# Kernel tuning notes

Measured on AMD Instinct MI355X. Metric: run time of the kernel, lower is better.

## Reference

```python
import jax, jax.numpy as jnp
import numpy as np

DIM = 2048
NUM_HEADS = 16
HEAD_DIM = DIM // NUM_HEADS  # 128
LATENT = 512
THETA = 10000.0


def rotate_half(x):
    # interleaved rotate: (x0,x1,x2,x3,...) -> (-x1,x0,-x3,x2,...)
    x1 = x[..., ::2]
    x2 = x[..., 1::2]
    return jnp.stack((-x2, x1), axis=-1).reshape(x.shape)


def apply_rope(x, sin, cos):
    return x * cos + rotate_half(x) * sin


def setup_inputs() -> dict:
    key = jax.random.key(0)
    ks = jax.random.split(key, 6)
    s_in = 1.0 / np.sqrt(DIM)
    s_lat = 1.0 / np.sqrt(LATENT)
    x = jax.random.normal(ks[0], (2, 2048, DIM), dtype=jnp.float32)
    Wq = jax.random.normal(ks[1], (DIM, DIM), dtype=jnp.float32) * s_in
    Wdkv = jax.random.normal(ks[2], (DIM, 2 * LATENT), dtype=jnp.float32) * s_in
    Wuk = jax.random.normal(ks[3], (LATENT, DIM), dtype=jnp.float32) * s_lat
    Wuv = jax.random.normal(ks[4], (LATENT, DIM), dtype=jnp.float32) * s_lat
    Wo = jax.random.normal(ks[5], (DIM, DIM), dtype=jnp.float32) * s_in
    return {"x": x, "Wq": Wq, "Wdkv": Wdkv, "Wuk": Wuk, "Wuv": Wuv, "Wo": Wo}


def reference(x, Wq, Wdkv, Wuk, Wuv, Wo):
    b, s, _ = x.shape
    # q projection -> [b, h, s, hd]
    q = (x @ Wq).reshape(b, s, NUM_HEADS, HEAD_DIM).transpose(0, 2, 1, 3)
    # low-rank latent down-projection, then up-project K and V
    dkv = x @ Wdkv  # [b, s, 2*L]
    dk, dv = dkv[..., :LATENT], dkv[..., LATENT:]
    k = (dk @ Wuk).reshape(b, s, NUM_HEADS, HEAD_DIM).transpose(0, 2, 1, 3)
    v = (dv @ Wuv).reshape(b, s, NUM_HEADS, HEAD_DIM).transpose(0, 2, 1, 3)
    # RoPE cache (concatenated freqs, matching the torch module)
    inv_freq = 1.0 / (THETA ** (jnp.arange(0, HEAD_DIM, 2, dtype=jnp.float32) / HEAD_DIM))
    t = jnp.arange(s, dtype=jnp.float32)
    freqs = t[:, None] * inv_freq[None, :]          # [s, hd/2]
    emb = jnp.concatenate([freqs, freqs], axis=-1)  # [s, hd]
    sin, cos = jnp.sin(emb), jnp.cos(emb)
    q = apply_rope(q, sin, cos)
    k = apply_rope(k, sin, cos)
    # SDPA (no mask, no dropout): scale = 1/sqrt(head_dim)
    scores = jnp.einsum('bhqd,bhkd->bhqk', q, k) / jnp.sqrt(jnp.float32(HEAD_DIM))
    attn = jax.nn.softmax(scores, axis=-1)
    out = jnp.einsum('bhqk,bhkd->bhqd', attn, v)
    out = out.transpose(0, 2, 1, 3).reshape(b, s, DIM)
    return out @ Wo
```

## Files before the change

### kernel.cpp

```cpp
#include <hip/hip_runtime.h>
#include <hip/hip_bf16.h>
#include <stdint.h>

typedef __attribute__((ext_vector_type(8))) __bf16 bf16x8;
typedef __attribute__((ext_vector_type(4))) float f32x4;

__device__ __forceinline__ unsigned short f2bf(float f) {
  union { float f; unsigned u; } v; v.f = f;
  unsigned r = v.u + 0x7FFFu + ((v.u >> 16) & 1u);
  return (unsigned short)(r >> 16);
}

__device__ __forceinline__ float fast_exp2(float x) {
#if __has_builtin(__builtin_amdgcn_exp2f)
  return __builtin_amdgcn_exp2f(x);
#else
  return exp2f(x);
#endif
}

__device__ __forceinline__ void gload_lds16(const void* g, void* l) {
  __builtin_amdgcn_global_load_lds((const __attribute__((address_space(1))) void*)g,
                                   (__attribute__((address_space(3))) void*)l,
                                   16, 0, 0);
}

__global__ __launch_bounds__(256) void k_prep(
    const float* __restrict__ x, unsigned short* __restrict__ xb,
    const float* __restrict__ Wq, unsigned short* __restrict__ WqT,
    const float* __restrict__ Wdkv, unsigned short* __restrict__ WdkvT,
    const float* __restrict__ Wuk, unsigned short* __restrict__ WukT,
    const float* __restrict__ Wuv, unsigned short* __restrict__ WuvT,
    float* __restrict__ cosT, float* __restrict__ sinT) {
  const int bid = blockIdx.x;
  const int tid = threadIdx.x;
  if (bid < 8192) {
    int i = (bid * 256 + tid) * 4;
    float4 v = *reinterpret_cast<const float4*>(x + i);
    ushort4 o;
    o.x = f2bf(v.x); o.y = f2bf(v.y); o.z = f2bf(v.z); o.w = f2bf(v.w);
    *reinterpret_cast<ushort4*>(xb + i) = o;
    return;
  }
  if (bid >= 16384) {
    int idx = (bid - 16384) * 256 + tid;
    int t = idx >> 6, j = idx & 63;
    float inv = powf(10000.f, -(float)j / 64.f);
    float ang = (float)t * inv;
    cosT[idx] = cosf(ang);
    sinT[idx] = sinf(ang);
    return;
  }
  const float* in; unsigned short* out; int K, N, lid;
  if (bid < 12288)      { in = Wq;   out = WqT;   K = 2048; N = 2048; lid = bid - 8192; }
  else if (bid < 14336) { in = Wdkv; out = WdkvT; K = 2048; N = 1024; lid = bid - 12288; }
  else if (bid < 15360) { in = Wuk;  out = WukT;  K = 512;  N = 2048; lid = bid - 14336; }
  else                  { in = Wuv;  out = WuvT;  K = 512;  N = 2048; lid = bid - 15360; }
  const int ntx = N >> 5;
  const int nt = lid % ntx, kt = lid / ntx;
  __shared__ float t[32][33];
  const int tx = tid & 31, ty = tid >> 5;
#pragma unroll
  for (int i = 0; i < 4; i++)
    t[ty + i * 8][tx] = in[(size_t)(kt * 32 + ty + i * 8) * N + nt * 32 + tx];
  __syncthreads();
#pragma unroll
  for (int i = 0; i < 4; i++)
    out[(size_t)(nt * 32 + ty + i * 8) * K + kt * 32 + tx] = f2bf(t[tx][ty + i * 8]);
}

template <int EPI>
__global__ __launch_bounds__(256, 2) void k_gemm(
    const unsigned short* __restrict__ A, int lda,
    const unsigned short* __restrict__ BT, int ldb,
    void* __restrict__ Cout, void* __restrict__ Cout2, int M, int N, int K,
    const float* __restrict__ cosT, const float* __restrict__ sinT) {
  __shared__ __attribute__((aligned(16))) unsigned short As[128 * 64];
  __shared__ __attribute__((aligned(16))) unsigned short Bs[128 * 64];
  const int tid = threadIdx.x;

  if (EPI == 3 && blockIdx.y >= 32) {
    const float* Win = cosT;
    unsigned short* Wout = (unsigned short*)Cout2;
    float (*t)[33] = (float(*)[33])As;
    const int tx = tid & 31, ty = tid >> 5;
    const int lid = (blockIdx.y - 32) * gridDim.x + blockIdx.x;
    for (int it = 0; it < 128; ++it) {
      int tile = lid * 128 + it;
      int nt = tile & 63, kt2 = tile >> 6;
#pragma unroll
      for (int i = 0; i < 4; i++)
        t[ty + i * 8][tx] = Win[(size_t)(kt2 * 32 + ty + i * 8) * 2048 + nt * 32 + tx];
      __syncthreads();
#pragma unroll
      for (int i = 0; i < 4; i++)
        Wout[(size_t)(nt * 32 + ty + i * 8) * 2048 + kt2 * 32 + tx] = f2bf(t[tx][ty + i * 8]);
      __syncthreads();
    }
    return;
  }

  const int lane = tid & 63;
  const int w = tid >> 6;
  const int wr = w >> 1, wc = w & 1;

  const int nby = (EPI == 3) ? 32 : gridDim.y;
  const int nwg = gridDim.x * nby;
  const int cpx = nwg >> 3;
  int flat = blockIdx.y * gridDim.x + blockIdx.x;
  flat = (flat & 7) * cpx + (flat >> 3);
  const int m0 = (flat / gridDim.x) * 128, n0 = (flat % gridDim.x) * 128;

  f32x4 acc[4][4] = {};

  const int srow = w * 8 + (lane >> 3);
  const int sch = (lane & 7) * 8;
  const unsigned short* gA = A + (size_t)(m0 + srow) * lda + sch;
  const unsigned short* gB = BT + (size_t)(n0 + srow) * ldb + sch;
  unsigned short* lA = &As[srow * 64 + sch];
  unsigned short* lB = &Bs[srow * 64 + sch];

  for (int kt = 0; kt < K; kt += 64) {
    __syncthreads();
#pragma unroll
    for (int i = 0; i < 4; i++) {
      gload_lds16(gA + (size_t)(i * 32) * lda + kt, lA + i * 32 * 64);
      gload_lds16(gB + (size_t)(i * 32) * ldb + kt, lB + i * 32 * 64);
    }
    __syncthreads();
#pragma unroll
    for (int kk = 0; kk < 64; kk += 32) {
      bf16x8 af[4], bfr[4];
#pragma unroll
      for (int m = 0; m < 4; m++)
        af[m] = *reinterpret_cast<const bf16x8*>(&As[(wr * 64 + m * 16 + (lane & 15)) * 64 + kk + (lane >> 4) * 8]);
#pragma unroll
      for (int n = 0; n < 4; n++)
        bfr[n] = *reinterpret_cast<const bf16x8*>(&Bs[(wc * 64 + n * 16 + (lane & 15)) * 64 + kk + (lane >> 4) * 8]);
#pragma unroll
      for (int m = 0; m < 4; m++)
#pragma unroll
        for (int n = 0; n < 4; n++) {
          if (EPI == 3)
            acc[m][n] = __builtin_amdgcn_mfma_f32_16x16x32_bf16(bfr[n], af[m], acc[m][n], 0, 0, 0);
          else
            acc[m][n] = __builtin_amdgcn_mfma_f32_16x16x32_bf16(af[m], bfr[n], acc[m][n], 0, 0, 0);
        }
    }
  }

  const int rl = (lane >> 4) * 4;
  const int cl = lane & 15;
#pragma unroll
  for (int m = 0; m < 4; m++)
#pragma unroll
    for (int n = 0; n < 4; n++)
#pragma unroll
      for (int r = 0; r < 4; r++) {
        float v = acc[m][n][r];
        if (EPI == 4) {
          int gr = m0 + wr * 64 + m * 16 + rl + r;
          int gc = n0 + wc * 64 + n * 16 + cl;
          ((float*)Cout)[(size_t)gr * N + gc] = v;
        } else if (EPI == 1) {
          int gr = m0 + wr * 64 + m * 16 + rl + r;
          int gc = n0 + wc * 64 + n * 16 + cl;
          int b = gr >> 11, s = gr & 2047, h = gc >> 7, d = gc & 127;
          float p = __shfl_xor(v, 1);
          float c = cosT[s * 64 + (d & 63)];
          float sn = sinT[s * 64 + (d & 63)];
          v = v * c + ((d & 1) ? p : -p) * sn;
          ((unsigned short*)Cout)[((size_t)(b * 16 + h) * 2048 + s) * 128 + d] = f2bf(v);
        } else if (EPI == 5) {
          int gr = m0 + wr * 64 + m * 16 + rl + r;
          int gc = n0 + wc * 64 + n * 16 + cl;
          if (n0 < 2048) {
            int b = gr >> 11, s = gr & 2047, h = gc >> 7, d = gc & 127;
            float p = __shfl_xor(v, 1);
            float c = cosT[s * 64 + (d & 63)];
            float sn = sinT[s * 64 + (d & 63)];
            v = v * c + ((d & 1) ? p : -p) * sn;
            ((unsigned short*)Cout)[((size_t)(b * 16 + h) * 2048 + s) * 128 + d] = f2bf(v);
          } else {
            ((unsigned short*)Cout2)[(size_t)gr * 1024 + (gc - 2048)] = f2bf(v);
          }
        } else {
          int gd = n0 + wc * 64 + n * 16 + rl + r;
          int gs = m0 + wr * 64 + m * 16 + cl;
          int b = gs >> 11, s = gs & 2047, h = gd >> 7, d = gd & 127;
          ((unsigned short*)Cout)[((size_t)(b * 16 + h) * 128 + d) * 2048 + s] = f2bf(v);
        }
      }
}

__global__ __launch_bounds__(256, 2) void k_attn(
    const unsigned short* __restrict__ Q,
    const unsigned short* __restrict__ Kt,
    const unsigned short* __restrict__ Vt,
    unsigned short* __restrict__ O) {
  __shared__ __attribute__((aligned(16))) unsigned short Kls[2][64 * 128];
  __shared__ __attribute__((aligned(16))) unsigned short Vls[2][128 * 64];
  __shared__ __attribute__((aligned(16))) unsigned short Pls[128 * 64];
  const int flat = blockIdx.x + (blockIdx.y << 4);
  const int swz = (flat & 7) * 64 + (flat >> 3);
  const int qt = swz & 15, bh = swz >> 4;
  const int tid = threadIdx.x, lane = tid & 63, w = tid >> 6;
  const unsigned short* Qh = Q + (size_t)bh * 2048 * 128;
  const unsigned short* Kh = Kt + (size_t)bh * 2048 * 128;
  const unsigned short* Vh = Vt + (size_t)bh * 128 * 2048;
  const int q0 = qt * 128;

  bf16x8 qf[2][4];
#pragma unroll
  for (int m = 0; m < 2; m++)
#pragma unroll
    for (int kd = 0; kd < 4; kd++) {
      int row = q0 + w * 32 + m * 16 + (lane & 15);
      int k = kd * 32 + (lane >> 4) * 8;
      qf[m][kd] = *reinterpret_cast<const bf16x8*>(Qh + (size_t)row * 128 + k);
    }

  f32x4 accO[2][8] = {};
  float lsum[2] = {0.f, 0.f};

  const int kr0 = w * 4 + (lane >> 4);
  const int kcb = lane & 15;
  const int vr0 = w * 8 + (lane >> 3);
  const int vcb = lane & 7;

  auto stage = [&](int buf, int kt) {
#pragma unroll
    for (int i = 0; i < 4; i++) {
      int rr = kr0 + i * 16;
      gload_lds16(Kh + (size_t)(kt * 64 + rr) * 128 + ((kcb ^ (rr & 7)) * 8),
                  (char*)Kls + buf * 16384 + rr * 256 + kcb * 16);
    }
#pragma unroll
    for (int i = 0; i < 4; i++) {
      int rr = vr0 + i * 32;
      gload_lds16(Vh + (size_t)rr * 2048 + kt * 64 + ((vcb ^ (rr & 7)) * 8),
                  (char*)Vls + buf * 16384 + rr * 128 + vcb * 16);
    }
  };

  stage(0, 0);
  __syncthreads();

  const float CL2 = 0.08838834764831845f * 1.44269504088896f;

  for (int kt = 0; kt < 32; kt++) {
    const int cur = kt & 1;
    if (kt + 1 < 32) stage(cur ^ 1, kt + 1);

    f32x4 accT[4][2] = {};
#pragma unroll
    for (int kd = 0; kd < 4; kd++) {
      bf16x8 kf[4];
#pragma unroll
      for (int n = 0; n < 4; n++) {
        int row = n * 16 + (lane & 15);
        int byte = cur * 16384 + row * 256 + (((kd * 32 + (lane >> 4) * 8) * 2) ^ ((row & 7) << 4));
        kf[n] = *reinterpret_cast<const bf16x8*>((const char*)Kls + byte);
      }
      __builtin_amdgcn_s_setprio(1);
#pragma unroll
      for (int n = 0; n < 4; n++)
#pragma unroll
        for (int m = 0; m < 2; m++)
          accT[n][m] = __builtin_amdgcn_mfma_f32_16x16x32_bf16(kf[n], qf[m][kd], accT[n][m], 0, 0, 0);
      __builtin_amdgcn_s_setprio(0);
    }

#pragma unroll
    for (int n = 0; n < 4; n++)
#pragma unroll
      for (int m = 0; m < 2; m++) {
        float p0 = fast_exp2(accT[n][m][0] * CL2);
        float p1 = fast_exp2(accT[n][m][1] * CL2);
        float p2 = fast_exp2(accT[n][m][2] * CL2);
        float p3 = fast_exp2(accT[n][m][3] * CL2);
        lsum[m] += (p0 + p1) + (p2 + p3);
        unsigned pk0, pk1;
        asm("v_cvt_pk_bf16_f32 %0, %1, %2" : "=v"(pk0) : "v"(p0), "v"(p1));
        asm("v_cvt_pk_bf16_f32 %0, %1, %2" : "=v"(pk1) : "v"(p2), "v"(p3));
        int row = w * 32 + m * 16 + (lane & 15);
        int kcol = n * 16 + (lane >> 4) * 4;
        int byte = row * 128 + ((kcol * 2) ^ ((row & 7) << 4));
        uint2 pk = {pk0, pk1};
        *reinterpret_cast<uint2*>((char*)Pls + byte) = pk;
      }

#pragma unroll
    for (int kk = 0; kk < 2; kk++) {
      bf16x8 pf[2], vf[8];
#pragma unroll
      for (int m = 0; m < 2; m++) {
        int row = w * 32 + m * 16 + (lane & 15);
        int byte = row * 128 + (((kk * 32 + (lane >> 4) * 8) * 2) ^ ((row & 7) << 4));
        pf[m] = *reinterpret_cast<const bf16x8*>((const char*)Pls + byte);
      }
#pragma unroll
      for (int n = 0; n < 8; n++) {
        int row = n * 16 + (lane & 15);
        int byte = cur * 16384 + row * 128 + (((kk * 32 + (lane >> 4) * 8) * 2) ^ ((row & 7) << 4));
        vf[n] = *reinterpret_cast<const bf16x8*>((const char*)Vls + byte);
      }
      __builtin_amdgcn_s_setprio(1);
#pragma unroll
      for (int m = 0; m < 2; m++)
#pragma unroll
        for (int n = 0; n < 8; n++)
          accO[m][n] = __builtin_amdgcn_mfma_f32_16x16x32_bf16(pf[m], vf[n], accO[m][n], 0, 0, 0);
      __builtin_amdgcn_s_setprio(0);
    }

    __syncthreads();
  }

  const int rl = (lane >> 4) * 4;
  float rv[2][4];
#pragma unroll
  for (int m = 0; m < 2; m++) {
    float s = lsum[m];
    s += __shfl_xor(s, 16);
    s += __shfl_xor(s, 32);
    float inv = 1.0f / s;
#pragma unroll
    for (int r = 0; r < 4; r++) rv[m][r] = __shfl(inv, rl + r);
  }

  const int b = bh >> 4, h = bh & 15;
#pragma unroll
  for (int m = 0; m < 2; m++)
#pragma unroll
    for (int n = 0; n < 8; n++)
#pragma unroll
      for (int r = 0; r < 4; r++) {
        int s = q0 + w * 32 + m * 16 + rl + r;
        int d = n * 16 + (lane & 15);
        O[((size_t)(b * 2048 + s)) * 2048 + h * 128 + d] = f2bf(accO[m][n][r] * rv[m][r]);
      }
}


extern "C" void kernel_launch(void* const* d_in, const int* in_sizes, int n_in,
                              void* d_out, int out_size, void* d_ws, size_t ws_size,
                              hipStream_t stream) {
  const float* x    = (const float*)d_in[0];
  const float* Wq   = (const float*)d_in[1];
  const float* Wdkv = (const float*)d_in[2];
  const float* Wuk  = (const float*)d_in[3];
  const float* Wuv  = (const float*)d_in[4];
  const float* Wo   = (const float*)d_in[5];

  char* ws = (char*)d_ws;
  unsigned short* xb    = (unsigned short*)(ws + 0);
  unsigned short* WqT   = (unsigned short*)(ws + 16777216);
  unsigned short* WdkvT = (unsigned short*)(ws + 25165824);
  unsigned short* WukT  = (unsigned short*)(ws + 29360128);
  unsigned short* WuvT  = (unsigned short*)(ws + 31457280);
  unsigned short* dkv   = (unsigned short*)(ws + 33554432);
  unsigned short* q_att = (unsigned short*)(ws + 41943040);
  unsigned short* k_att = (unsigned short*)(ws + 58720256);
  unsigned short* vT    = (unsigned short*)(ws + 75497472);
  float* cosT           = (float*)(ws + 92274688);
  float* sinT           = (float*)(ws + 92798976);

  k_prep<<<16896, 256, 0, stream>>>(x, xb, Wq, WqT, Wdkv, WdkvT, Wuk, WukT, Wuv, WuvT, cosT, sinT);

  k_gemm<5><<<dim3(24, 32), 256, 0, stream>>>(xb, 2048, WqT, 2048, q_att, dkv, 4096, 3072, 2048, cosT, sinT);
  k_gemm<1><<<dim3(16, 32), 256, 0, stream>>>(dkv, 1024, WukT, 512, k_att, nullptr, 4096, 2048, 512, cosT, sinT);
  k_gemm<3><<<dim3(16, 34), 256, 0, stream>>>(dkv + 512, 1024, WuvT, 512, vT, WqT, 4096, 2048, 512, Wo, nullptr);
  k_attn<<<dim3(16, 32), 256, 0, stream>>>(q_att, k_att, vT, xb);
  k_gemm<4><<<dim3(16, 32), 256, 0, stream>>>(xb, 2048, WqT, 2048, (float*)d_out, nullptr, 4096, 2048, 2048, nullptr, nullptr);
}
```

Measured before the change: 308.9 us.

## Merge K and V up-projection GEMMs and Wo transpose into one launch

```diff
diff --git a/kernel.cpp b/kernel.cpp
--- a/kernel.cpp
+++ b/kernel.cpp
@@ -74,27 +74,27 @@
     const unsigned short* __restrict__ A, int lda,
     const unsigned short* __restrict__ BT, int ldb,
     void* __restrict__ Cout, void* __restrict__ Cout2, int M, int N, int K,
-    const float* __restrict__ cosT, const float* __restrict__ sinT) {
+    const float* __restrict__ cosT, const float* __restrict__ sinT,
+    const unsigned short* __restrict__ X1, const float* __restrict__ X2,
+    unsigned short* __restrict__ X3) {
   __shared__ __attribute__((aligned(16))) unsigned short As[128 * 64];
   __shared__ __attribute__((aligned(16))) unsigned short Bs[128 * 64];
   const int tid = threadIdx.x;
 
-  if (EPI == 3 && blockIdx.y >= 32) {
-    const float* Win = cosT;
-    unsigned short* Wout = (unsigned short*)Cout2;
+  if (EPI == 6 && blockIdx.x >= 1024) {
     float (*t)[33] = (float(*)[33])As;
     const int tx = tid & 31, ty = tid >> 5;
-    const int lid = (blockIdx.y - 32) * gridDim.x + blockIdx.x;
-    for (int it = 0; it < 128; ++it) {
-      int tile = lid * 128 + it;
+#pragma unroll
+    for (int it = 0; it < 4; ++it) {
+      int tile = (blockIdx.x - 1024) * 4 + it;
       int nt = tile & 63, kt2 = tile >> 6;
 #pragma unroll
       for (int i = 0; i < 4; i++)
-        t[ty + i * 8][tx] = Win[(size_t)(kt2 * 32 + ty + i * 8) * 2048 + nt * 32 + tx];
+        t[ty + i * 8][tx] = X2[(size_t)(kt2 * 32 + ty + i * 8) * 2048 + nt * 32 + tx];
       __syncthreads();
 #pragma unroll
       for (int i = 0; i < 4; i++)
-        Wout[(size_t)(nt * 32 + ty + i * 8) * 2048 + kt2 * 32 + tx] = f2bf(t[tx][ty + i * 8]);
+        X3[(size_t)(nt * 32 + ty + i * 8) * 2048 + kt2 * 32 + tx] = f2bf(t[tx][ty + i * 8]);
       __syncthreads();
     }
     return;
@@ -104,19 +104,28 @@
   const int w = tid >> 6;
   const int wr = w >> 1, wc = w & 1;
 
-  const int nby = (EPI == 3) ? 32 : gridDim.y;
-  const int nwg = gridDim.x * nby;
-  const int cpx = nwg >> 3;
-  int flat = blockIdx.y * gridDim.x + blockIdx.x;
-  flat = (flat & 7) * cpx + (flat >> 3);
-  const int m0 = (flat / gridDim.x) * 128, n0 = (flat % gridDim.x) * 128;
+  const unsigned short* Ap = A; int ldA = lda;
+  const unsigned short* Bp = BT; int ldB = ldb;
+  int m0, n0; bool vmode = false;
+  if (EPI == 6) {
+    const int bid = blockIdx.x;
+    if (bid < 512) { m0 = (bid >> 4) * 128; n0 = (bid & 15) * 128; }
+    else {
+      vmode = true;
+      Ap = X1; ldA = 512; Bp = A + 512; ldB = 1024;
+      const int b2 = bid - 512;
+      m0 = (b2 & 15) * 128; n0 = (b2 >> 4) * 128;
+    }
+  } else {
+    m0 = blockIdx.y * 128; n0 = blockIdx.x * 128;
+  }
 
   f32x4 acc[4][4] = {};
 
   const int srow = w * 8 + (lane >> 3);
   const int sch = (lane & 7) * 8;
-  const unsigned short* gA = A + (size_t)(m0 + srow) * lda + sch;
-  const unsigned short* gB = BT + (size_t)(n0 + srow) * ldb + sch;
+  const unsigned short* gA = Ap + (size_t)(m0 + srow) * ldA + sch;
+  const unsigned short* gB = Bp + (size_t)(n0 + srow) * ldB + sch;
   unsigned short* lA = &As[srow * 64 + sch];
   unsigned short* lB = &Bs[srow * 64 + sch];
 
@@ -124,8 +133,8 @@
     __syncthreads();
 #pragma unroll
     for (int i = 0; i < 4; i++) {
-      gload_lds16(gA + (size_t)(i * 32) * lda + kt, lA + i * 32 * 64);
-      gload_lds16(gB + (size_t)(i * 32) * ldb + kt, lB + i * 32 * 64);
+      gload_lds16(gA + (size_t)(i * 32) * ldA + kt, lA + i * 32 * 64);
+      gload_lds16(gB + (size_t)(i * 32) * ldB + kt, lB + i * 32 * 64);
     }
     __syncthreads();
 #pragma unroll
@@ -140,12 +149,8 @@
 #pragma unroll
       for (int m = 0; m < 4; m++)
 #pragma unroll
-        for (int n = 0; n < 4; n++) {
-          if (EPI == 3)
-            acc[m][n] = __builtin_amdgcn_mfma_f32_16x16x32_bf16(bfr[n], af[m], acc[m][n], 0, 0, 0);
-          else
-            acc[m][n] = __builtin_amdgcn_mfma_f32_16x16x32_bf16(af[m], bfr[n], acc[m][n], 0, 0, 0);
-        }
+        for (int n = 0; n < 4; n++)
+          acc[m][n] = __builtin_amdgcn_mfma_f32_16x16x32_bf16(af[m], bfr[n], acc[m][n], 0, 0, 0);
     }
   }
 
@@ -158,13 +163,11 @@
 #pragma unroll
       for (int r = 0; r < 4; r++) {
         float v = acc[m][n][r];
+        int gr = m0 + wr * 64 + m * 16 + rl + r;
+        int gc = n0 + wc * 64 + n * 16 + cl;
         if (EPI == 4) {
-          int gr = m0 + wr * 64 + m * 16 + rl + r;
-          int gc = n0 + wc * 64 + n * 16 + cl;
           ((float*)Cout)[(size_t)gr * N + gc] = v;
         } else if (EPI == 1) {
-          int gr = m0 + wr * 64 + m * 16 + rl + r;
-          int gc = n0 + wc * 64 + n * 16 + cl;
           int b = gr >> 11, s = gr & 2047, h = gc >> 7, d = gc & 127;
           float p = __shfl_xor(v, 1);
           float c = cosT[s * 64 + (d & 63)];
@@ -172,8 +175,6 @@
           v = v * c + ((d & 1) ? p : -p) * sn;
           ((unsigned short*)Cout)[((size_t)(b * 16 + h) * 2048 + s) * 128 + d] = f2bf(v);
         } else if (EPI == 5) {
-          int gr = m0 + wr * 64 + m * 16 + rl + r;
-          int gc = n0 + wc * 64 + n * 16 + cl;
           if (n0 < 2048) {
             int b = gr >> 11, s = gr & 2047, h = gc >> 7, d = gc & 127;
             float p = __shfl_xor(v, 1);
@@ -185,10 +186,17 @@
             ((unsigned short*)Cout2)[(size_t)gr * 1024 + (gc - 2048)] = f2bf(v);
           }
         } else {
-          int gd = n0 + wc * 64 + n * 16 + rl + r;
-          int gs = m0 + wr * 64 + m * 16 + cl;
-          int b = gs >> 11, s = gs & 2047, h = gd >> 7, d = gd & 127;
-          ((unsigned short*)Cout)[((size_t)(b * 16 + h) * 128 + d) * 2048 + s] = f2bf(v);
+          if (!vmode) {
+            int b = gr >> 11, s = gr & 2047, h = gc >> 7, d = gc & 127;
+            float p = __shfl_xor(v, 1);
+            float c = cosT[s * 64 + (d & 63)];
+            float sn = sinT[s * 64 + (d & 63)];
+            v = v * c + ((d & 1) ? p : -p) * sn;
+            ((unsigned short*)Cout)[((size_t)(b * 16 + h) * 2048 + s) * 128 + d] = f2bf(v);
+          } else {
+            int h = gr >> 7, d = gr & 127, b = gc >> 11, s = gc & 2047;
+            ((unsigned short*)Cout2)[(((size_t)(b * 16 + h) * 128) + d) * 2048 + s] = f2bf(v);
+          }
         }
       }
 }
@@ -368,9 +376,11 @@
 
   k_prep<<<16896, 256, 0, stream>>>(x, xb, Wq, WqT, Wdkv, WdkvT, Wuk, WukT, Wuv, WuvT, cosT, sinT);
 
-  k_gemm<5><<<dim3(24, 32), 256, 0, stream>>>(xb, 2048, WqT, 2048, q_att, dkv, 4096, 3072, 2048, cosT, sinT);
-  k_gemm<1><<<dim3(16, 32), 256, 0, stream>>>(dkv, 1024, WukT, 512, k_att, nullptr, 4096, 2048, 512, cosT, sinT);
-  k_gemm<3><<<dim3(16, 34), 256, 0, stream>>>(dkv + 512, 1024, WuvT, 512, vT, WqT, 4096, 2048, 512, Wo, nullptr);
+  k_gemm<5><<<dim3(24, 32), 256, 0, stream>>>(xb, 2048, WqT, 2048, q_att, dkv, 4096, 3072, 2048,
+                                              cosT, sinT, nullptr, nullptr, nullptr);
+  k_gemm<6><<<2048, 256, 0, stream>>>(dkv, 1024, WukT, 512, k_att, vT, 4096, 2048, 512,
+                                      cosT, sinT, WuvT, Wo, WqT);
   k_attn<<<dim3(16, 32), 256, 0, stream>>>(q_att, k_att, vT, xb);
-  k_gemm<4><<<dim3(16, 32), 256, 0, stream>>>(xb, 2048, WqT, 2048, (float*)d_out, nullptr, 4096, 2048, 2048, nullptr, nullptr);
-}
+  k_gemm<4><<<dim3(16, 32), 256, 0, stream>>>(xb, 2048, WqT, 2048, (float*)d_out, nullptr, 4096, 2048, 2048,
+                                              nullptr, nullptr, nullptr, nullptr, nullptr);
+}
```

Measured after the change: 247.8 us. 19.8% less time.
